# Kernel optimization log

Hardware: AMD Instinct MI355X
Metric: run time of the kernel (lower is better)

The kernel has to match this reference:

```python
import jax, jax.numpy as jnp
import numpy as np
import math

IN_DIM = 3
WIDTH = 256
DEPTH = 6
OUT_DIM = 1
W0_FIRST = 30.0
W0_HIDDEN = 1.0
N_POINTS = 1048576


def _uniform(key, shape, bound):
    return jax.random.uniform(key, shape, dtype=jnp.float32, minval=-bound, maxval=bound)


def setup_inputs() -> dict:
    key = jax.random.key(0)
    ks = jax.random.split(key, 8)
    xyt = jax.random.uniform(ks[0], (N_POINTS, IN_DIM), dtype=jnp.float32, minval=-1.0, maxval=1.0)
    # first layer: bound = 1/in_features
    W0 = _uniform(ks[1], (WIDTH, IN_DIM), 1.0 / IN_DIM)
    b0 = jnp.zeros((WIDTH,), jnp.float32)
    # hidden layers: bound = sqrt(6/width)/w0_hidden
    hb = math.sqrt(6.0 / WIDTH) / W0_HIDDEN
    W1 = _uniform(ks[2], (WIDTH, WIDTH), hb)
    b1 = jnp.zeros((WIDTH,), jnp.float32)
    W2 = _uniform(ks[3], (WIDTH, WIDTH), hb)
    b2 = jnp.zeros((WIDTH,), jnp.float32)
    W3 = _uniform(ks[4], (WIDTH, WIDTH), hb)
    b3 = jnp.zeros((WIDTH,), jnp.float32)
    W4 = _uniform(ks[5], (WIDTH, WIDTH), hb)
    b4 = jnp.zeros((WIDTH,), jnp.float32)
    Wf = _uniform(ks[6], (OUT_DIM, WIDTH), hb)
    bf = jnp.zeros((OUT_DIM,), jnp.float32)
    return {"xyt": xyt, "W0": W0, "b0": b0, "W1": W1, "b1": b1,
            "W2": W2, "b2": b2, "W3": W3, "b3": b3, "W4": W4, "b4": b4,
            "Wf": Wf, "bf": bf}


def reference(xyt, W0, b0, W1, b1, W2, b2, W3, b3, W4, b4, Wf, bf):
    # SineLayer: sin(w0 * (x @ W^T + b)); torch Linear weight is [out, in]
    h = jnp.sin(W0_FIRST * (xyt @ W0.T + b0))          # [N, 256]
    for W, b in ((W1, b1), (W2, b2), (W3, b3), (W4, b4)):
        h = jnp.sin(W0_HIDDEN * (h @ W.T + b))          # [N, 256]
    out = h @ Wf.T + bf                                  # [N, 1]
    return out.squeeze(-1)                               # [N]
```

## Files before the change

### kernel.cpp

```cpp
#include <hip/hip_runtime.h>

typedef _Float16 half8 __attribute__((ext_vector_type(8)));
typedef _Float16 half4 __attribute__((ext_vector_type(4)));
typedef float f32x4 __attribute__((ext_vector_type(4)));

#define NPB 128
#define THREADS 512
#define INV2PI 0.15915494309189535f
#define W0SCALE (30.0f * INV2PI)
#define SMEM_BYTES (NPB * 256 * 2 + (384 + 256) * 4)

__device__ __forceinline__ int hswz(int row, int col) {
    return (row << 8) + (col ^ ((row & 7) << 3));
}

__global__ void convert_weights(const float* __restrict__ W1, const float* __restrict__ W2,
                                const float* __restrict__ W3, const float* __restrict__ W4,
                                _Float16* __restrict__ Wc) {
    int tid = blockIdx.x * 256 + threadIdx.x;
    int l   = tid >> 16;
    int rem = tid & 65535;
    int n = rem >> 8, k = rem & 255;
    const float* W = (l == 0) ? W1 : (l == 1) ? W2 : (l == 2) ? W3 : W4;
    int kc = k >> 5, kl = k & 31;
    Wc[l * 65536 + kc * 8192 + n * 32 + kl] = (_Float16)(W[rem] * INV2PI);
}

__launch_bounds__(THREADS, 4)
__global__ void siren_fused(const float* __restrict__ xyt,
                            const float* __restrict__ W0,
                            const float* __restrict__ b0,
                            const _Float16* __restrict__ Wc,
                            const float* __restrict__ b1,
                            const float* __restrict__ b2,
                            const float* __restrict__ b3,
                            const float* __restrict__ b4,
                            const float* __restrict__ Wf,
                            const float* __restrict__ bfin,
                            float* __restrict__ out)
{
    extern __shared__ _Float16 smem[];
    _Float16* hbuf = smem;
    float* xs   = (float*)(smem + NPB * 256);
    float* wf_s = xs + 384;

    const int tid  = threadIdx.x;
    const int lane = tid & 63;
    const int wv   = tid >> 6;
    const int pg   = wv >> 2;
    const int fb   = (wv & 3) << 6;
    const int l15  = lane & 15;
    const int l4   = lane >> 4;
    const int gm0  = blockIdx.x * NPB;

    if (tid < 384) xs[tid] = xyt[gm0 * 3 + tid];
    if (tid < 256) wf_s[tid] = Wf[tid];
    __syncthreads();

    {
        const int fg = lane;
        const int p0 = wv * 16;
        float w[4][3], bb[4];
        #pragma unroll
        for (int c = 0; c < 4; ++c) {
            const int n = fg * 4 + c;
            w[c][0] = W0[n * 3 + 0] * W0SCALE;
            w[c][1] = W0[n * 3 + 1] * W0SCALE;
            w[c][2] = W0[n * 3 + 2] * W0SCALE;
            bb[c]   = b0[n] * W0SCALE;
        }
        #pragma unroll 4
        for (int p = 0; p < 16; ++p) {
            const float x0 = xs[(p0 + p) * 3], x1 = xs[(p0 + p) * 3 + 1], x2 = xs[(p0 + p) * 3 + 2];
            half4 hv;
            #pragma unroll
            for (int c = 0; c < 4; ++c) {
                float z = fmaf(w[c][0], x0, fmaf(w[c][1], x1, fmaf(w[c][2], x2, bb[c])));
                hv[c] = (_Float16)__builtin_amdgcn_sinf(z);
            }
            *(half4*)&hbuf[hswz(p0 + p, fg * 4)] = hv;
        }
    }

    const int arow = (fb + l15) * 32 + l4 * 8;

    #pragma unroll
    for (int l = 0; l < 4; ++l) {
        const float* bl = (l == 0) ? b1 : (l == 1) ? b2 : (l == 2) ? b3 : b4;
        const _Float16* wl = Wc + l * 65536;

        half8 areg[2][4];
        #pragma unroll
        for (int i = 0; i < 4; ++i)
            areg[0][i] = *(const half8*)&wl[arow + i * 512];

        f32x4 acc[4][4];
        #pragma unroll
        for (int i = 0; i < 4; ++i) {
            f32x4 bb = *(const f32x4*)&bl[fb + i * 16 + l4 * 4];
            bb *= INV2PI;
            #pragma unroll
            for (int j = 0; j < 4; ++j)
                acc[i][j] = bb;
        }

        __syncthreads();

        #pragma unroll 2
        for (int kc = 0; kc < 8; ++kc) {
            const int cur = kc & 1, nxt = cur ^ 1;
            if (kc < 7) {
                #pragma unroll
                for (int i = 0; i < 4; ++i)
                    areg[nxt][i] = *(const half8*)&wl[(kc + 1) * 8192 + arow + i * 512];
            }
            #pragma unroll
            for (int g = 0; g < 2; ++g) {
                half8 bfr[2];
                #pragma unroll
                for (int j = 0; j < 2; ++j)
                    bfr[j] = *(const half8*)&hbuf[hswz(pg * 64 + (g * 2 + j) * 16 + l15,
                                                       kc * 32 + l4 * 8)];
                #pragma unroll
                for (int i = 0; i < 4; ++i)
                    #pragma unroll
                    for (int j = 0; j < 2; ++j)
                        acc[i][g * 2 + j] = __builtin_amdgcn_mfma_f32_16x16x32_f16(
                            areg[cur][i], bfr[j], acc[i][g * 2 + j], 0, 0, 0);
            }
        }

        __syncthreads();

        #pragma unroll
        for (int i = 0; i < 4; ++i)
            #pragma unroll
            for (int j = 0; j < 4; ++j) {
                half4 hv;
                #pragma unroll
                for (int r = 0; r < 4; ++r)
                    hv[r] = (_Float16)__builtin_amdgcn_sinf(acc[i][j][r]);
                *(half4*)&hbuf[hswz(pg * 64 + j * 16 + l15, fb + i * 16 + l4 * 4)] = hv;
            }
    }

    __syncthreads();

    {
        const int m = tid >> 2, q = tid & 3;
        float sum = 0.f;
        #pragma unroll
        for (int i = 0; i < 8; ++i) {
            half8 hv = *(const half8*)&hbuf[hswz(m, q * 64 + i * 8)];
            const int nb = q * 64 + i * 8;
            #pragma unroll
            for (int j = 0; j < 8; ++j)
                sum = fmaf((float)hv[j], wf_s[nb + j], sum);
        }
        sum += __shfl_down(sum, 2);
        sum += __shfl_down(sum, 1);
        if (q == 0) out[gm0 + m] = sum + bfin[0];
    }
}

extern "C" void kernel_launch(void* const* d_in, const int* in_sizes, int n_in,
                              void* d_out, int out_size, void* d_ws, size_t ws_size,
                              hipStream_t stream) {
    const float* xyt = (const float*)d_in[0];
    const float* W0  = (const float*)d_in[1];
    const float* b0  = (const float*)d_in[2];
    const float* W1  = (const float*)d_in[3];
    const float* b1  = (const float*)d_in[4];
    const float* W2  = (const float*)d_in[5];
    const float* b2  = (const float*)d_in[6];
    const float* W3  = (const float*)d_in[7];
    const float* b3  = (const float*)d_in[8];
    const float* W4  = (const float*)d_in[9];
    const float* b4  = (const float*)d_in[10];
    const float* Wf  = (const float*)d_in[11];
    const float* bf  = (const float*)d_in[12];
    float* out = (float*)d_out;
    _Float16* Wc = (_Float16*)d_ws;

    hipFuncSetAttribute((const void*)siren_fused,
                        hipFuncAttributeMaxDynamicSharedMemorySize, SMEM_BYTES);

    convert_weights<<<1024, 256, 0, stream>>>(W1, W2, W3, W4, Wc);

    const int N = in_sizes[0] / 3;
    siren_fused<<<N / NPB, THREADS, SMEM_BYTES, stream>>>(
        xyt, W0, b0, Wc, b1, b2, b3, b4, Wf, bf, out);
}
```

Baseline: 711.1 us.

## Shrink point tile to 96 and double-buffer LDS activation fragments in registers

Reduces points per block from 128 to 96, cutting LDS use per block so more blocks can be resident per CU. Each wave now handles 48 points, using 4x3 MFMA accumulator tiles. The K loop is fully unrolled, both weight chunks are preloaded, and activation fragments are double-buffered in registers to overlap LDS reads with MFMAs. Bounds checks and a ceil-div grid are added because N is not a multiple of 96. The trade-off is more weight-fetch traffic per point.

```diff
diff --git a/kernel.cpp b/kernel.cpp
--- a/kernel.cpp
+++ b/kernel.cpp
@@ -4,11 +4,11 @@
 typedef _Float16 half4 __attribute__((ext_vector_type(4)));
 typedef float f32x4 __attribute__((ext_vector_type(4)));
 
-#define NPB 128
+#define NPB 96
 #define THREADS 512
 #define INV2PI 0.15915494309189535f
 #define W0SCALE (30.0f * INV2PI)
-#define SMEM_BYTES (NPB * 256 * 2 + (384 + 256) * 4)
+#define SMEM_BYTES (NPB * 256 * 2 + (288 + 256) * 4)
 
 __device__ __forceinline__ int hswz(int row, int col) {
     return (row << 8) + (col ^ ((row & 7) << 3));
@@ -37,12 +37,13 @@
                             const float* __restrict__ b4,
                             const float* __restrict__ Wf,
                             const float* __restrict__ bfin,
-                            float* __restrict__ out)
+                            float* __restrict__ out,
+                            int npts)
 {
     extern __shared__ _Float16 smem[];
     _Float16* hbuf = smem;
     float* xs   = (float*)(smem + NPB * 256);
-    float* wf_s = xs + 384;
+    float* wf_s = xs + 288;
 
     const int tid  = threadIdx.x;
     const int lane = tid & 63;
@@ -52,14 +53,15 @@
     const int l15  = lane & 15;
     const int l4   = lane >> 4;
     const int gm0  = blockIdx.x * NPB;
-
-    if (tid < 384) xs[tid] = xyt[gm0 * 3 + tid];
+    const int nv   = min(NPB, npts - gm0);
+
+    if (tid < 288) xs[tid] = (tid < nv * 3) ? xyt[gm0 * 3 + tid] : 0.f;
     if (tid < 256) wf_s[tid] = Wf[tid];
     __syncthreads();
 
     {
         const int fg = lane;
-        const int p0 = wv * 16;
+        const int p0 = wv * 12;
         float w[4][3], bb[4];
         #pragma unroll
         for (int c = 0; c < 4; ++c) {
@@ -70,7 +72,7 @@
             bb[c]   = b0[n] * W0SCALE;
         }
         #pragma unroll 4
-        for (int p = 0; p < 16; ++p) {
+        for (int p = 0; p < 12; ++p) {
             const float x0 = xs[(p0 + p) * 3], x1 = xs[(p0 + p) * 3 + 1], x2 = xs[(p0 + p) * 3 + 2];
             half4 hv;
             #pragma unroll
@@ -91,42 +93,62 @@
 
         half8 areg[2][4];
         #pragma unroll
-        for (int i = 0; i < 4; ++i)
-            areg[0][i] = *(const half8*)&wl[arow + i * 512];
-
-        f32x4 acc[4][4];
+        for (int c = 0; c < 2; ++c)
+            #pragma unroll
+            for (int i = 0; i < 4; ++i)
+                areg[c][i] = *(const half8*)&wl[c * 8192 + arow + i * 512];
+
+        f32x4 acc[4][3];
         #pragma unroll
         for (int i = 0; i < 4; ++i) {
             f32x4 bb = *(const f32x4*)&bl[fb + i * 16 + l4 * 4];
             bb *= INV2PI;
             #pragma unroll
-            for (int j = 0; j < 4; ++j)
+            for (int j = 0; j < 3; ++j)
                 acc[i][j] = bb;
         }
 
         __syncthreads();
 
-        #pragma unroll 2
-        for (int kc = 0; kc < 8; ++kc) {
-            const int cur = kc & 1, nxt = cur ^ 1;
-            if (kc < 7) {
+        half8 bfrA[3], bfrB[3];
+        #pragma unroll
+        for (int j = 0; j < 3; ++j)
+            bfrA[j] = *(const half8*)&hbuf[hswz(pg * 48 + j * 16 + l15, l4 * 8)];
+
+        #pragma unroll
+        for (int kcp = 0; kcp < 4; ++kcp) {
+            const int kc = 2 * kcp;
+            #pragma unroll
+            for (int j = 0; j < 3; ++j)
+                bfrB[j] = *(const half8*)&hbuf[hswz(pg * 48 + j * 16 + l15,
+                                                   (kc + 1) * 32 + l4 * 8)];
+            #pragma unroll
+            for (int i = 0; i < 4; ++i)
+                #pragma unroll
+                for (int j = 0; j < 3; ++j)
+                    acc[i][j] = __builtin_amdgcn_mfma_f32_16x16x32_f16(
+                        areg[0][i], bfrA[j], acc[i][j], 0, 0, 0);
+            if (kcp < 3) {
                 #pragma unroll
                 for (int i = 0; i < 4; ++i)
-                    areg[nxt][i] = *(const half8*)&wl[(kc + 1) * 8192 + arow + i * 512];
-            }
-            #pragma unroll
-            for (int g = 0; g < 2; ++g) {
-                half8 bfr[2];
-                #pragma unroll
-                for (int j = 0; j < 2; ++j)
-                    bfr[j] = *(const half8*)&hbuf[hswz(pg * 64 + (g * 2 + j) * 16 + l15,
-                                                       kc * 32 + l4 * 8)];
+                    areg[0][i] = *(const half8*)&wl[(kc + 2) * 8192 + arow + i * 512];
+            }
+            if (kcp < 3) {
+                #pragma unroll
+                for (int j = 0; j < 3; ++j)
+                    bfrA[j] = *(const half8*)&hbuf[hswz(pg * 48 + j * 16 + l15,
+                                                       (kc + 2) * 32 + l4 * 8)];
+            }
+            #pragma unroll
+            for (int i = 0; i < 4; ++i)
+                #pragma unroll
+                for (int j = 0; j < 3; ++j)
+                    acc[i][j] = __builtin_amdgcn_mfma_f32_16x16x32_f16(
+                        areg[1][i], bfrB[j], acc[i][j], 0, 0, 0);
+            if (kcp < 3) {
                 #pragma unroll
                 for (int i = 0; i < 4; ++i)
-                    #pragma unroll
-                    for (int j = 0; j < 2; ++j)
-                        acc[i][g * 2 + j] = __builtin_amdgcn_mfma_f32_16x16x32_f16(
-                            areg[cur][i], bfr[j], acc[i][g * 2 + j], 0, 0, 0);
+                    areg[1][i] = *(const half8*)&wl[(kc + 3) * 8192 + arow + i * 512];
             }
         }
 
@@ -135,12 +157,12 @@
         #pragma unroll
         for (int i = 0; i < 4; ++i)
             #pragma unroll
-            for (int j = 0; j < 4; ++j) {
+            for (int j = 0; j < 3; ++j) {
                 half4 hv;
                 #pragma unroll
                 for (int r = 0; r < 4; ++r)
                     hv[r] = (_Float16)__builtin_amdgcn_sinf(acc[i][j][r]);
-                *(half4*)&hbuf[hswz(pg * 64 + j * 16 + l15, fb + i * 16 + l4 * 4)] = hv;
+                *(half4*)&hbuf[hswz(pg * 48 + j * 16 + l15, fb + i * 16 + l4 * 4)] = hv;
             }
     }
 
@@ -148,18 +170,20 @@
 
     {
         const int m = tid >> 2, q = tid & 3;
-        float sum = 0.f;
-        #pragma unroll
-        for (int i = 0; i < 8; ++i) {
-            half8 hv = *(const half8*)&hbuf[hswz(m, q * 64 + i * 8)];
-            const int nb = q * 64 + i * 8;
-            #pragma unroll
-            for (int j = 0; j < 8; ++j)
-                sum = fmaf((float)hv[j], wf_s[nb + j], sum);
-        }
-        sum += __shfl_down(sum, 2);
-        sum += __shfl_down(sum, 1);
-        if (q == 0) out[gm0 + m] = sum + bfin[0];
+        if (m < nv) {
+            float sum = 0.f;
+            #pragma unroll
+            for (int i = 0; i < 8; ++i) {
+                half8 hv = *(const half8*)&hbuf[hswz(m, q * 64 + i * 8)];
+                const int nb = q * 64 + i * 8;
+                #pragma unroll
+                for (int j = 0; j < 8; ++j)
+                    sum = fmaf((float)hv[j], wf_s[nb + j], sum);
+            }
+            sum += __shfl_down(sum, 2);
+            sum += __shfl_down(sum, 1);
+            if (q == 0) out[gm0 + m] = sum + bfin[0];
+        }
     }
 }
 
@@ -188,6 +212,7 @@
     convert_weights<<<1024, 256, 0, stream>>>(W1, W2, W3, W4, Wc);
 
     const int N = in_sizes[0] / 3;
-    siren_fused<<<N / NPB, THREADS, SMEM_BYTES, stream>>>(
-        xyt, W0, b0, Wc, b1, b2, b3, b4, Wf, bf, out);
-}
+    const int grid = (N + NPB - 1) / NPB;
+    siren_fused<<<grid, THREADS, SMEM_BYTES, stream>>>(
+        xyt, W0, b0, Wc, b1, b2, b3, b4, Wf, bf, out, N);
+}
```

Measured after the change: 827.1 us. 1.16x slower.
